# Performance work log

Measured on AMD Instinct MI355X. Metric: run time of the kernel, lower is better.

Reference implementation:

```python
import jax, jax.numpy as jnp
import numpy as np

EMBED_DIM = 1024
HEADS = 16
HEAD_DIM = EMBED_DIM // HEADS


def setup_inputs() -> dict:
    key = jax.random.key(0)
    ks = jax.random.split(key, 5)
    B, N, C = 2, 2048, EMBED_DIM
    scale = 1.0 / np.sqrt(C)
    x = jax.random.normal(ks[0], (B, N, C), dtype=jnp.float32)
    W_qkv = jax.random.normal(ks[1], (C, 3 * C), dtype=jnp.float32) * scale
    b_qkv = jax.random.normal(ks[2], (3 * C,), dtype=jnp.float32) * 0.01
    W_out = jax.random.normal(ks[3], (C, C), dtype=jnp.float32) * scale
    b_out = jax.random.normal(ks[4], (C,), dtype=jnp.float32) * 0.01
    return {"x": x, "W_qkv": W_qkv, "b_qkv": b_qkv, "W_out": W_out, "b_out": b_out}


def reference(x, W_qkv, b_qkv, W_out, b_out):
    B, N, C = x.shape
    qkv = x @ W_qkv + b_qkv                      # [B, N, 3C]
    qkv = qkv.reshape(B, N, 3, HEADS, HEAD_DIM)
    qkv = jnp.transpose(qkv, (2, 0, 3, 1, 4))    # [3, B, H, N, d]
    q, k, v = qkv[0], qkv[1], qkv[2]
    attn = jnp.einsum('bhnd,bhmd->bhnm', q, k) / np.sqrt(HEAD_DIM)
    attn = jax.nn.softmax(attn, axis=-1)
    out = jnp.einsum('bhnm,bhmd->bhnd', attn, v)  # [B, H, N, d]
    out = jnp.transpose(out, (0, 2, 1, 3)).reshape(B, N, C)
    return out @ W_out + b_out
```

## Files before the change

### kernel.cpp

```cpp
#include <hip/hip_runtime.h>
#include <stdint.h>

typedef __bf16 bf16_t;
typedef bf16_t bf16x8 __attribute__((ext_vector_type(8)));
typedef bf16_t bf16x2v __attribute__((ext_vector_type(2)));
typedef short short4v __attribute__((ext_vector_type(4)));
typedef float f32x4 __attribute__((ext_vector_type(4)));
typedef uint32_t u32x2 __attribute__((ext_vector_type(2)));

#define BATCH 2
#define SEQ 2048
#define CDIM 1024
#define NH 16
#define HD 64

#define QSCALE 0.18033688011f

__device__ __forceinline__ uint16_t f32_bf16(float f) {
    __bf16 h = (__bf16)f;
    return __builtin_bit_cast(uint16_t, h);
}

__device__ __forceinline__ uint32_t pack_bf16(float a, float b) {
    bf16x2v t;
    t.x = (__bf16)a;
    t.y = (__bf16)b;
    return __builtin_bit_cast(uint32_t, t);
}

__device__ __forceinline__ bf16x8 ld8(const uint16_t* p) {
    return *reinterpret_cast<const bf16x8*>(p);
}

__device__ __forceinline__ void gld16(const uint16_t* g, uint16_t* l) {
    __builtin_amdgcn_global_load_lds(
        (__attribute__((address_space(1))) void*)(g),
        (__attribute__((address_space(3))) void*)(l), 16, 0, 0);
}

#define LDS_FENCE() asm volatile("s_waitcnt lgkmcnt(0)" ::: "memory")

__global__ __launch_bounds__(256) void prep_kernel(
        const float* __restrict__ x, uint16_t* __restrict__ x_bf,
        const float* __restrict__ Wqkv, uint16_t* __restrict__ wqkvT,
        const float* __restrict__ Wout, uint16_t* __restrict__ woutT) {
    const int bid = blockIdx.x, tid = threadIdx.x;
    if (bid < 4096) {
        int i = (bid * 256 + tid) * 4;
        float4 v = *(const float4*)(x + i);
        ushort4 o;
        o.x = f32_bf16(v.x);
        o.y = f32_bf16(v.y);
        o.z = f32_bf16(v.z);
        o.w = f32_bf16(v.w);
        *(ushort4*)(x_bf + i) = o;
        return;
    }
    __shared__ float tile[32][33];
    const float* in;
    uint16_t* outp;
    int idx, Cc, ncx;
    if (bid < 4096 + 3072) { idx = bid - 4096; in = Wqkv; outp = wqkvT; Cc = 3072; ncx = 96; }
    else                   { idx = bid - 7168; in = Wout; outp = woutT; Cc = 1024; ncx = 32; }
    const int R = 1024;
    int bx = idx % ncx, by = idx / ncx;
    int c0 = bx * 32, r0 = by * 32;
    int tx = tid & 31, ty = tid >> 5;
#pragma unroll
    for (int i = 0; i < 4; i++)
        tile[ty + i * 8][tx] = in[(size_t)(r0 + ty + i * 8) * Cc + c0 + tx];
    __syncthreads();
    const int rr = tid >> 3, seg = tid & 7;
    ushort4 o;
    o.x = f32_bf16(tile[seg * 4 + 0][rr]);
    o.y = f32_bf16(tile[seg * 4 + 1][rr]);
    o.z = f32_bf16(tile[seg * 4 + 2][rr]);
    o.w = f32_bf16(tile[seg * 4 + 3][rr]);
    *(ushort4*)(outp + (size_t)(c0 + rr) * R + r0 + seg * 4) = o;
}

template <int BM, int BN, int MODE>
__global__ __launch_bounds__(256) void gemm_t(
        const uint16_t* __restrict__ A, const uint16_t* __restrict__ Bt, int K,
        const float* __restrict__ bias,
        uint16_t* __restrict__ qw, uint16_t* __restrict__ kw, uint16_t* __restrict__ vt,
        float* __restrict__ out) {
    constexpr int WT_M = BM / 2, WT_N = BN / 2;
    constexpr int MI = WT_M / 16, NJ = WT_N / 16;
    constexpr int ASEG_W = BM / 64, BSEG_W = BN / 64;
    constexpr int AB = 2 * BM * 32 + 2 * BN * 32;
    constexpr int TS = (MODE == 0) ? 4 * 64 * 68 : 0;
    constexpr int SM = AB > TS ? AB : TS;
    __shared__ uint16_t smem[SM];
    uint16_t* As = smem;
    uint16_t* Bs = smem + 2 * BM * 32;

    const int m0 = blockIdx.y * BM, n0 = blockIdx.x * BN;
    const int tid = threadIdx.x;
    const int w = tid >> 6, lane = tid & 63;
    const int quad = lane >> 4, l16 = lane & 15;
    const int wm = (w >> 1) * WT_M, wn = (w & 1) * WT_N;

    const int srow = lane >> 2;
    const int schunk = (lane & 3) ^ (srow & 3);

    const uint16_t* aP[ASEG_W];
    const uint16_t* bP[BSEG_W];
    int aL[ASEG_W], bL[BSEG_W];
#pragma unroll
    for (int s = 0; s < ASEG_W; s++) {
        int seg = w * ASEG_W + s;
        aP[s] = A + (size_t)(m0 + seg * 16 + srow) * K + schunk * 8;
        aL[s] = seg * 512;
    }
#pragma unroll
    for (int s = 0; s < BSEG_W; s++) {
        int seg = w * BSEG_W + s;
        bP[s] = Bt + (size_t)(n0 + seg * 16 + srow) * K + schunk * 8;
        bL[s] = seg * 512;
    }

    auto stage = [&](int buf, int k0) {
#pragma unroll
        for (int s = 0; s < ASEG_W; s++) gld16(aP[s] + k0, As + buf * BM * 32 + aL[s]);
#pragma unroll
        for (int s = 0; s < BSEG_W; s++) gld16(bP[s] + k0, Bs + buf * BN * 32 + bL[s]);
    };

    const int cslot = (quad ^ (l16 & 3)) * 8;
    f32x4 acc[MI][NJ] = {};

    stage(0, 0);
    const int iters = K / 32;
    for (int it = 0; it < iters; ++it) {
        __syncthreads();
        if (it + 1 < iters) stage((it + 1) & 1, (it + 1) * 32);
        const uint16_t* A_ = As + (it & 1) * BM * 32;
        const uint16_t* B_ = Bs + (it & 1) * BN * 32;
        bf16x8 af[MI], bfr[NJ];
#pragma unroll
        for (int i = 0; i < MI; i++) af[i] = ld8(&A_[(wm + i * 16 + l16) * 32 + cslot]);
#pragma unroll
        for (int j = 0; j < NJ; j++) bfr[j] = ld8(&B_[(wn + j * 16 + l16) * 32 + cslot]);
#pragma unroll
        for (int i = 0; i < MI; i++)
#pragma unroll
            for (int j = 0; j < NJ; j++)
                acc[i][j] = __builtin_amdgcn_mfma_f32_16x16x32_bf16(af[i], bfr[j], acc[i][j], 0, 0, 0);
    }

    const int nbase = n0 + wn;
    float bj[NJ];
#pragma unroll
    for (int j = 0; j < NJ; j++) bj[j] = bias[nbase + j * 16 + l16];

    if constexpr (MODE == 1) {
#pragma unroll
        for (int j = 0; j < NJ; j++) {
#pragma unroll
            for (int i = 0; i < MI; i++)
#pragma unroll
                for (int r = 0; r < 4; r++) {
                    int m = m0 + wm + i * 16 + quad * 4 + r;
                    out[(size_t)m * CDIM + nbase + j * 16 + l16] = acc[i][j][r] + bj[j];
                }
        }
    } else {
        __syncthreads();
        uint16_t* T = smem + w * 64 * 68;
        const int gmb = m0 + wm;
        const int b = gmb >> 11, ns0 = gmb & 2047;

        if (nbase < 2048) {
            const int which = nbase >> 10, h = (nbase & 1023) >> 6;
            const float sc = (which == 0) ? QSCALE : 1.0f;
#pragma unroll
            for (int i = 0; i < 4; i++)
#pragma unroll
                for (int j = 0; j < 4; j++)
#pragma unroll
                    for (int r = 0; r < 4; r++)
                        T[(i * 16 + quad * 4 + r) * 68 + j * 16 + l16] =
                            f32_bf16((acc[i][j][r] + bj[j]) * sc);
            LDS_FENCE();
            uint16_t* dst = ((which == 0) ? qw : kw) +
                            (((size_t)b * NH + h) * SEQ + ns0 + lane) * HD;
#pragma unroll
            for (int g = 0; g < 8; g++) {
                bf16x8 v = ld8(&T[lane * 68 + g * 8]);
                *(bf16x8*)(dst + g * 8) = v;
            }
        } else {
#pragma unroll
            for (int i = 0; i < 4; i++)
#pragma unroll
                for (int j = 0; j < 4; j++) {
                    u32x2 pr;
                    pr.x = pack_bf16(acc[i][j][0] + bj[j], acc[i][j][1] + bj[j]);
                    pr.y = pack_bf16(acc[i][j][2] + bj[j], acc[i][j][3] + bj[j]);
                    *(u32x2*)&T[(j * 16 + l16) * 68 + i * 16 + quad * 4] = pr;
                }
            LDS_FENCE();
            const int h = (nbase - 2048) >> 6;
            uint16_t* dst = vt + (((size_t)b * NH + h) * HD + lane) * SEQ + ns0;
#pragma unroll
            for (int g = 0; g < 16; g++) {
                u32x2 d2 = *(const u32x2*)&T[lane * 68 + g * 4];
                int npos = (g & 3) * 16 + (g >> 2) * 4;
                *(u32x2*)(dst + npos) = d2;
            }
        }
    }
}

__global__ __launch_bounds__(256) void attn_kernel(
        const uint16_t* __restrict__ qg, const uint16_t* __restrict__ kg,
        const uint16_t* __restrict__ vt, uint16_t* __restrict__ og) {
    __shared__ uint16_t Ks[2][128 * 64];
    __shared__ uint16_t Vs[2][64 * 128];

    const int bh = blockIdx.x;
    const int qt = blockIdx.y;
    const int tid = threadIdx.x;
    const int w = tid >> 6, lane = tid & 63;
    const int quad = lane >> 4, l16 = lane & 15;
    const int qrow0 = qt * 128 + w * 32;
    const size_t base = (size_t)bh * SEQ * HD;

    bf16x8 qf[2][2];
#pragma unroll
    for (int mg = 0; mg < 2; mg++)
#pragma unroll
        for (int ks = 0; ks < 2; ks++)
            qf[mg][ks] = ld8(qg + base + (size_t)(qrow0 + mg * 16 + l16) * HD + ks * 32 + quad * 8);

    const int krow = lane >> 3;
    const int kch = (lane & 7) ^ krow;
    const int vrow = lane >> 4;
    const uint16_t* ksrc[4];
    const uint16_t* vsrc[4];
#pragma unroll
    for (int s = 0; s < 4; s++) {
        int seg = w * 4 + s;
        ksrc[s] = kg + base + (size_t)(seg * 8 + krow) * HD + kch * 8;
        int vd = seg * 4 + vrow;
        int vch = (lane & 15) ^ (vd & 15);
        vsrc[s] = vt + base + (size_t)vd * SEQ + vch * 8;
    }

    f32x4 o_acc[2][4] = {};
    f32x4 l_acc[2] = {};
    const short4v ones = { (short)0x3F80, (short)0x3F80, (short)0x3F80, (short)0x3F80 };

    auto stage = [&](int buf) {
#pragma unroll
        for (int s = 0; s < 4; s++) {
            int seg = w * 4 + s;
            gld16(ksrc[s], &Ks[buf][seg * 512]);
            ksrc[s] += 128 * HD;
        }
#pragma unroll
        for (int s = 0; s < 4; s++) {
            int seg = w * 4 + s;
            gld16(vsrc[s], &Vs[buf][seg * 512]);
            vsrc[s] += 128;
        }
    };

    stage(0);

    const int NT = SEQ / 128;
    for (int it = 0; it < NT; ++it) {
        __syncthreads();
        if (it + 1 < NT) stage((it + 1) & 1);
        const uint16_t* K_ = Ks[it & 1];
        const uint16_t* V_ = Vs[it & 1];

#pragma unroll
        for (int sub = 0; sub < 2; sub++) {
            f32x4 S[2][4] = {};
#pragma unroll
            for (int nf = 0; nf < 4; nf++) {
                const int krow_rd = (sub * 64 + nf * 16 + l16) * 64;
#pragma unroll
                for (int ks = 0; ks < 2; ks++) {
                    bf16x8 kf = ld8(&K_[krow_rd + (((ks * 4 + quad) ^ (l16 & 7)) * 8)]);
#pragma unroll
                    for (int mg = 0; mg < 2; mg++)
                        S[mg][nf] = __builtin_amdgcn_mfma_f32_16x16x32_bf16(kf, qf[mg][ks], S[mg][nf], 0, 0, 0);
                }
            }

            uint32_t pk[2][4][2];
#pragma unroll
            for (int mg = 0; mg < 2; mg++)
#pragma unroll
                for (int nf = 0; nf < 4; nf++) {
                    float p0 = __builtin_amdgcn_exp2f(S[mg][nf][0]);
                    float p1 = __builtin_amdgcn_exp2f(S[mg][nf][1]);
                    float p2 = __builtin_amdgcn_exp2f(S[mg][nf][2]);
                    float p3 = __builtin_amdgcn_exp2f(S[mg][nf][3]);
                    pk[mg][nf][0] = pack_bf16(p0, p1);
                    pk[mg][nf][1] = pack_bf16(p2, p3);
                }

#pragma unroll
            for (int mg = 0; mg < 2; mg++)
#pragma unroll
                for (int kc = 0; kc < 4; kc++) {
                    short4v pfrag = __builtin_bit_cast(short4v, (u32x2){pk[mg][kc][0], pk[mg][kc][1]});
                    l_acc[mg] = __builtin_amdgcn_mfma_f32_16x16x16bf16_1k(ones, pfrag, l_acc[mg], 0, 0, 0);
                }

#pragma unroll
            for (int mf = 0; mf < 4; mf++) {
                const int dr = mf * 16 + l16;
                const int ro = dr * 128;
                const int c0 = (sub * 8 + quad * 2 + 0) ^ (dr & 15);
                const int c1 = (sub * 8 + quad * 2 + 1) ^ (dr & 15);
                uint4 v0 = *(const uint4*)&V_[ro + c0 * 8];
                uint4 v1 = *(const uint4*)&V_[ro + c1 * 8];
                short4v vf[4];
                vf[0] = __builtin_bit_cast(short4v, (u32x2){v0.x, v0.y});
                vf[1] = __builtin_bit_cast(short4v, (u32x2){v0.z, v0.w});
                vf[2] = __builtin_bit_cast(short4v, (u32x2){v1.x, v1.y});
                vf[3] = __builtin_bit_cast(short4v, (u32x2){v1.z, v1.w});
#pragma unroll
                for (int kc = 0; kc < 4; kc++)
#pragma unroll
                    for (int mg = 0; mg < 2; mg++) {
                        short4v pfrag = __builtin_bit_cast(short4v, (u32x2){pk[mg][kc][0], pk[mg][kc][1]});
                        o_acc[mg][mf] = __builtin_amdgcn_mfma_f32_16x16x16bf16_1k(vf[kc], pfrag, o_acc[mg][mf], 0, 0, 0);
                    }
            }
        }
    }

    const int b = bh >> 4, h = bh & 15;
#pragma unroll
    for (int mg = 0; mg < 2; mg++) {
        const float inv = __builtin_amdgcn_rcpf(l_acc[mg][0]);
        const int ns = qrow0 + mg * 16 + l16;
        uint16_t* orow = og + (((size_t)b * SEQ + ns) * NH + h) * HD + quad * 4;
#pragma unroll
        for (int mf = 0; mf < 4; mf++) {
            ushort4 o;
            o.x = f32_bf16(o_acc[mg][mf][0] * inv);
            o.y = f32_bf16(o_acc[mg][mf][1] * inv);
            o.z = f32_bf16(o_acc[mg][mf][2] * inv);
            o.w = f32_bf16(o_acc[mg][mf][3] * inv);
            *(ushort4*)(orow + mf * 16) = o;
        }
    }
}

extern "C" void kernel_launch(void* const* d_in, const int* in_sizes, int n_in,
                              void* d_out, int out_size, void* d_ws, size_t ws_size,
                              hipStream_t stream) {
    const float* x = (const float*)d_in[0];
    const float* Wqkv = (const float*)d_in[1];
    const float* bqkv = (const float*)d_in[2];
    const float* Wout = (const float*)d_in[3];
    const float* bout = (const float*)d_in[4];
    float* out = (float*)d_out;

    uint16_t* ws = (uint16_t*)d_ws;
    uint16_t* x_bf  = ws;
    uint16_t* wqkvT = x_bf + 4194304;
    uint16_t* woutT = wqkvT + 3145728;
    uint16_t* qw    = woutT + 1048576;
    uint16_t* kw    = qw + 4194304;
    uint16_t* vtw   = kw + 4194304;
    uint16_t* attn  = vtw + 4194304;

    prep_kernel<<<8192, 256, 0, stream>>>(x, x_bf, Wqkv, wqkvT, Wout, woutT);

    gemm_t<128, 128, 0><<<dim3(24, 32), 256, 0, stream>>>(
        x_bf, wqkvT, 1024, bqkv, qw, kw, vtw, nullptr);

    attn_kernel<<<dim3(32, 16), 256, 0, stream>>>(qw, kw, vtw, attn);

    gemm_t<64, 128, 1><<<dim3(8, 64), 256, 0, stream>>>(
        attn, woutT, 1024, bout, nullptr, nullptr, nullptr, out);
}
```

Measured before the change: 190.8 us.

## Switch attention to 32x32x16 MFMA tiles with permlane32 swap for P fragments

Rewrites the attention inner loop to use 32x32x16 bf16 MFMAs instead of 16x16 variants, for QK^T, the row-sum and PV. The P matrix is repacked between the S accumulator layout and the B-operand layout with v_permlane32_swap rather than going through LDS. The V-transpose layout written by the QKV kernel is changed to match the new fragment ordering. The aim is fewer MFMA issues and fewer LDS reads per unit of work, at the cost of larger accumulator register footprints and reliance on a gfx950 permlane instruction.

```diff
diff --git a/kernel.cpp b/kernel.cpp
--- a/kernel.cpp
+++ b/kernel.cpp
@@ -4,9 +4,10 @@
 typedef __bf16 bf16_t;
 typedef bf16_t bf16x8 __attribute__((ext_vector_type(8)));
 typedef bf16_t bf16x2v __attribute__((ext_vector_type(2)));
-typedef short short4v __attribute__((ext_vector_type(4)));
 typedef float f32x4 __attribute__((ext_vector_type(4)));
+typedef float f32x16 __attribute__((ext_vector_type(16)));
 typedef uint32_t u32x2 __attribute__((ext_vector_type(2)));
+typedef uint32_t u32x4 __attribute__((ext_vector_type(4)));
 
 #define BATCH 2
 #define SEQ 2048
@@ -30,6 +31,16 @@
 
 __device__ __forceinline__ bf16x8 ld8(const uint16_t* p) {
     return *reinterpret_cast<const bf16x8*>(p);
+}
+
+__device__ __forceinline__ void swap32(uint32_t& a, uint32_t& b) {
+#if __has_builtin(__builtin_amdgcn_permlane32_swap)
+    u32x2 r = __builtin_amdgcn_permlane32_swap(a, b, false, false);
+    a = r.x;
+    b = r.y;
+#else
+    asm("v_permlane32_swap_b32 %0, %1" : "+v"(a), "+v"(b));
+#endif
 }
 
 __device__ __forceinline__ void gld16(const uint16_t* g, uint16_t* l) {
@@ -206,8 +217,7 @@
 #pragma unroll
             for (int g = 0; g < 16; g++) {
                 u32x2 d2 = *(const u32x2*)&T[lane * 68 + g * 4];
-                int npos = (g & 3) * 16 + (g >> 2) * 4;
-                *(u32x2*)(dst + npos) = d2;
+                *(u32x2*)(dst + g * 4) = d2;
             }
         }
     }
@@ -223,16 +233,14 @@
     const int qt = blockIdx.y;
     const int tid = threadIdx.x;
     const int w = tid >> 6, lane = tid & 63;
-    const int quad = lane >> 4, l16 = lane & 15;
+    const int l32 = lane & 31, hi = lane >> 5;
     const int qrow0 = qt * 128 + w * 32;
     const size_t base = (size_t)bh * SEQ * HD;
 
-    bf16x8 qf[2][2];
-#pragma unroll
-    for (int mg = 0; mg < 2; mg++)
-#pragma unroll
-        for (int ks = 0; ks < 2; ks++)
-            qf[mg][ks] = ld8(qg + base + (size_t)(qrow0 + mg * 16 + l16) * HD + ks * 32 + quad * 8);
+    bf16x8 qf[4];
+#pragma unroll
+    for (int s = 0; s < 4; s++)
+        qf[s] = ld8(qg + base + (size_t)(qrow0 + l32) * HD + s * 16 + hi * 8);
 
     const int krow = lane >> 3;
     const int kch = (lane & 7) ^ krow;
@@ -248,9 +256,11 @@
         vsrc[s] = vt + base + (size_t)vd * SEQ + vch * 8;
     }
 
-    f32x4 o_acc[2][4] = {};
-    f32x4 l_acc[2] = {};
-    const short4v ones = { (short)0x3F80, (short)0x3F80, (short)0x3F80, (short)0x3F80 };
+    f32x16 o_acc[2] = {};
+    f32x16 l_acc = {};
+    u32x4 ov;
+    ov.x = 0x3F803F80u; ov.y = 0x3F803F80u; ov.z = 0x3F803F80u; ov.w = 0x3F803F80u;
+    const bf16x8 ones8 = __builtin_bit_cast(bf16x8, ov);
 
     auto stage = [&](int buf) {
 #pragma unroll
@@ -268,6 +278,9 @@
     };
 
     stage(0);
+
+    const int kxe = l32 & 7;
+    const int vxe = l32 & 15;
 
     const int NT = SEQ / 128;
     for (int it = 0; it < NT; ++it) {
@@ -277,81 +290,58 @@
         const uint16_t* V_ = Vs[it & 1];
 
 #pragma unroll
-        for (int sub = 0; sub < 2; sub++) {
-            f32x4 S[2][4] = {};
-#pragma unroll
-            for (int nf = 0; nf < 4; nf++) {
-                const int krow_rd = (sub * 64 + nf * 16 + l16) * 64;
-#pragma unroll
-                for (int ks = 0; ks < 2; ks++) {
-                    bf16x8 kf = ld8(&K_[krow_rd + (((ks * 4 + quad) ^ (l16 & 7)) * 8)]);
-#pragma unroll
-                    for (int mg = 0; mg < 2; mg++)
-                        S[mg][nf] = __builtin_amdgcn_mfma_f32_16x16x32_bf16(kf, qf[mg][ks], S[mg][nf], 0, 0, 0);
+        for (int kvb = 0; kvb < 4; kvb++) {
+            f32x16 S = {};
+            const uint16_t* Krow = K_ + (kvb * 32 + l32) * 64;
+#pragma unroll
+            for (int s = 0; s < 4; s++) {
+                bf16x8 kf = ld8(Krow + ((2 * s + hi) ^ kxe) * 8);
+                S = __builtin_amdgcn_mfma_f32_32x32x16_bf16(kf, qf[s], S, 0, 0, 0);
+            }
+
+            uint32_t pk0[4], pk1[4];
+#pragma unroll
+            for (int c = 0; c < 4; c++) {
+                pk0[c] = pack_bf16(__builtin_amdgcn_exp2f(S[4 * c + 0]),
+                                   __builtin_amdgcn_exp2f(S[4 * c + 1]));
+                pk1[c] = pack_bf16(__builtin_amdgcn_exp2f(S[4 * c + 2]),
+                                   __builtin_amdgcn_exp2f(S[4 * c + 3]));
+            }
+
+#pragma unroll
+            for (int cp = 0; cp < 2; cp++) {
+                uint32_t b0 = pk0[2 * cp], b2 = pk0[2 * cp + 1];
+                uint32_t b1 = pk1[2 * cp], b3 = pk1[2 * cp + 1];
+                swap32(b0, b2);
+                swap32(b1, b3);
+                u32x4 t;
+                t.x = b0; t.y = b1; t.z = b2; t.w = b3;
+                bf16x8 pb = __builtin_bit_cast(bf16x8, t);
+
+                l_acc = __builtin_amdgcn_mfma_f32_32x32x16_bf16(ones8, pb, l_acc, 0, 0, 0);
+#pragma unroll
+                for (int mf = 0; mf < 2; mf++) {
+                    int ch = (kvb * 4 + cp * 2 + hi) ^ vxe;
+                    bf16x8 vf = ld8(V_ + (mf * 32 + l32) * 128 + ch * 8);
+                    o_acc[mf] = __builtin_amdgcn_mfma_f32_32x32x16_bf16(vf, pb, o_acc[mf], 0, 0, 0);
                 }
             }
-
-            uint32_t pk[2][4][2];
-#pragma unroll
-            for (int mg = 0; mg < 2; mg++)
-#pragma unroll
-                for (int nf = 0; nf < 4; nf++) {
-                    float p0 = __builtin_amdgcn_exp2f(S[mg][nf][0]);
-                    float p1 = __builtin_amdgcn_exp2f(S[mg][nf][1]);
-                    float p2 = __builtin_amdgcn_exp2f(S[mg][nf][2]);
-                    float p3 = __builtin_amdgcn_exp2f(S[mg][nf][3]);
-                    pk[mg][nf][0] = pack_bf16(p0, p1);
-                    pk[mg][nf][1] = pack_bf16(p2, p3);
-                }
-
-#pragma unroll
-            for (int mg = 0; mg < 2; mg++)
-#pragma unroll
-                for (int kc = 0; kc < 4; kc++) {
-                    short4v pfrag = __builtin_bit_cast(short4v, (u32x2){pk[mg][kc][0], pk[mg][kc][1]});
-                    l_acc[mg] = __builtin_amdgcn_mfma_f32_16x16x16bf16_1k(ones, pfrag, l_acc[mg], 0, 0, 0);
-                }
-
-#pragma unroll
-            for (int mf = 0; mf < 4; mf++) {
-                const int dr = mf * 16 + l16;
-                const int ro = dr * 128;
-                const int c0 = (sub * 8 + quad * 2 + 0) ^ (dr & 15);
-                const int c1 = (sub * 8 + quad * 2 + 1) ^ (dr & 15);
-                uint4 v0 = *(const uint4*)&V_[ro + c0 * 8];
-                uint4 v1 = *(const uint4*)&V_[ro + c1 * 8];
-                short4v vf[4];
-                vf[0] = __builtin_bit_cast(short4v, (u32x2){v0.x, v0.y});
-                vf[1] = __builtin_bit_cast(short4v, (u32x2){v0.z, v0.w});
-                vf[2] = __builtin_bit_cast(short4v, (u32x2){v1.x, v1.y});
-                vf[3] = __builtin_bit_cast(short4v, (u32x2){v1.z, v1.w});
-#pragma unroll
-                for (int kc = 0; kc < 4; kc++)
-#pragma unroll
-                    for (int mg = 0; mg < 2; mg++) {
-                        short4v pfrag = __builtin_bit_cast(short4v, (u32x2){pk[mg][kc][0], pk[mg][kc][1]});
-                        o_acc[mg][mf] = __builtin_amdgcn_mfma_f32_16x16x16bf16_1k(vf[kc], pfrag, o_acc[mg][mf], 0, 0, 0);
-                    }
-            }
         }
     }
 
     const int b = bh >> 4, h = bh & 15;
-#pragma unroll
-    for (int mg = 0; mg < 2; mg++) {
-        const float inv = __builtin_amdgcn_rcpf(l_acc[mg][0]);
-        const int ns = qrow0 + mg * 16 + l16;
-        uint16_t* orow = og + (((size_t)b * SEQ + ns) * NH + h) * HD + quad * 4;
-#pragma unroll
-        for (int mf = 0; mf < 4; mf++) {
-            ushort4 o;
-            o.x = f32_bf16(o_acc[mg][mf][0] * inv);
-            o.y = f32_bf16(o_acc[mg][mf][1] * inv);
-            o.z = f32_bf16(o_acc[mg][mf][2] * inv);
-            o.w = f32_bf16(o_acc[mg][mf][3] * inv);
-            *(ushort4*)(orow + mf * 16) = o;
-        }
-    }
+    const float inv = __builtin_amdgcn_rcpf(l_acc[0]);
+    const int ns = qrow0 + l32;
+    uint16_t* orow = og + (((size_t)b * SEQ + ns) * NH + h) * HD;
+#pragma unroll
+    for (int mf = 0; mf < 2; mf++)
+#pragma unroll
+        for (int c = 0; c < 4; c++) {
+            u32x2 pr;
+            pr.x = pack_bf16(o_acc[mf][4 * c + 0] * inv, o_acc[mf][4 * c + 1] * inv);
+            pr.y = pack_bf16(o_acc[mf][4 * c + 2] * inv, o_acc[mf][4 * c + 3] * inv);
+            *(u32x2*)(orow + mf * 32 + c * 8 + hi * 4) = pr;
+        }
 }
 
 extern "C" void kernel_launch(void* const* d_in, const int* in_sizes, int n_in,
```

Measured after the change: 185.0 us. 1.03x faster.
